# Optimization experiments

Hardware: AMD Instinct MI355X
Metric: run time of the kernel (lower is better)

The kernel has to match this reference:

```python
import jax, jax.numpy as jnp
import numpy as np

B, N, D = 1, 65536, 1024
H = 512
R = 16  # num_regions
C = 2   # num_classes

def _gelu(x):
    return jax.nn.gelu(x, approximate=False)  # torch nn.GELU default is exact erf

def setup_inputs() -> dict:
    key = jax.random.key(0)
    ks = jax.random.split(key, 16)
    s = 0.02
    return {
        "embeddings": jax.random.normal(ks[0], (B, N, D), dtype=jnp.float32),
        # region_encoder: Linear(D,H) + GELU (dropout=0 in eval)
        "W1": jax.random.normal(ks[1], (D, H), dtype=jnp.float32) * s,
        "b1": jnp.zeros((H,), dtype=jnp.float32),
        # region_attention: Linear(H,H//2) -> tanh -> Linear(H//2,1)
        "Wa1": jax.random.normal(ks[2], (H, H // 2), dtype=jnp.float32) * s,
        "ba1": jnp.zeros((H // 2,), dtype=jnp.float32),
        "Wa2": jax.random.normal(ks[3], (H // 2, 1), dtype=jnp.float32) * s,
        "ba2": jnp.zeros((1,), dtype=jnp.float32),
        # slide_encoder: Linear(H,H) + GELU
        "Ws": jax.random.normal(ks[4], (H, H), dtype=jnp.float32) * s,
        "bs": jnp.zeros((H,), dtype=jnp.float32),
        # slide_attention
        "Wsa1": jax.random.normal(ks[5], (H, H // 2), dtype=jnp.float32) * s,
        "bsa1": jnp.zeros((H // 2,), dtype=jnp.float32),
        "Wsa2": jax.random.normal(ks[6], (H // 2, 1), dtype=jnp.float32) * s,
        "bsa2": jnp.zeros((1,), dtype=jnp.float32),
        # classifier: Linear(H,H//2) -> GELU -> Linear(H//2,C)
        "Wc1": jax.random.normal(ks[7], (H, H // 2), dtype=jnp.float32) * s,
        "bc1": jnp.zeros((H // 2,), dtype=jnp.float32),
        "Wc2": jax.random.normal(ks[8], (H // 2, C), dtype=jnp.float32) * s,
        "bc2": jnp.zeros((C,), dtype=jnp.float32),
    }

def reference(embeddings, W1, b1, Wa1, ba1, Wa2, ba2, Ws, bs, Wsa1, bsa1, Wsa2, bsa2, Wc1, bc1, Wc2, bc2):
    b, n, d = embeddings.shape
    m = n // R  # patches per region
    # coords=None path: region_ids[i] = i % R, so region r holds indices r, r+R, ...
    # Equivalent regrouping via reshape+transpose: (B, M, R, D) -> (B, R, M, D)
    x = embeddings.reshape(b, m, R, d).transpose(0, 2, 1, 3)
    # region encoder
    region_emb = _gelu(jnp.einsum('brmd,dh->brmh', x, W1) + b1)  # (B,R,M,H)
    # region attention pooling
    scores = jnp.einsum('brmk,ko->brmo', jnp.tanh(jnp.einsum('brmh,hk->brmk', region_emb, Wa1) + ba1), Wa2) + ba2  # (B,R,M,1)
    attn = jax.nn.softmax(scores, axis=2)
    region_features = jnp.sum(region_emb * attn, axis=2)  # (B,R,H)
    # slide encoder + attention pooling over regions
    slide_emb = _gelu(jnp.einsum('brh,hg->brg', region_features, Ws) + bs)  # (B,R,H)
    sattn = jnp.einsum('brk,ko->bro', jnp.tanh(jnp.einsum('brh,hk->brk', slide_emb, Wsa1) + bsa1), Wsa2) + bsa2  # (B,R,1)
    sweights = jax.nn.softmax(sattn, axis=1)
    slide_rep = jnp.sum(slide_emb * sweights, axis=1)  # (B,H)
    # classifier
    logits = _gelu(slide_rep @ Wc1 + bc1) @ Wc2 + bc2  # (B,C)
    return logits
```

## Files before the change

### kernel.cpp

```cpp
#include <hip/hip_runtime.h>

#define NTOK 65536
#define DIN  1024
#define H    512
#define HH   256
#define NREG 16
#define MPR  4096

__device__ __forceinline__ unsigned short f2bf(float f) {
  unsigned u = __float_as_uint(f);
  u += 0x7fffu + ((u >> 16) & 1u);
  return (unsigned short)(u >> 16);
}
__device__ __forceinline__ float bf2f(unsigned short s) {
  return __uint_as_float(((unsigned)s) << 16);
}
__device__ __forceinline__ float gelu_exact(float x) {
  return 0.5f * x * (1.0f + erff(x * 0.70710678118654752440f));
}

typedef __attribute__((ext_vector_type(8))) short shortx8;
typedef __attribute__((ext_vector_type(4))) float floatx4;

__device__ __forceinline__ void gl_lds16(const void* g, void* l) {
  __builtin_amdgcn_global_load_lds(
      (const __attribute__((address_space(1))) void*)g,
      (__attribute__((address_space(3))) void*)l, 16, 0, 0);
}

__global__ __launch_bounds__(256) void kc_convert(const float* __restrict__ X,
                                                  unsigned short* __restrict__ Xb) {
  size_t i = ((size_t)blockIdx.x * 256 + threadIdx.x) * 8;
  const floatx4* src = (const floatx4*)(X + i);
  floatx4 f0 = src[0], f1 = src[1];
  shortx8 h;
  h[0] = (short)f2bf(f0[0]); h[1] = (short)f2bf(f0[1]);
  h[2] = (short)f2bf(f0[2]); h[3] = (short)f2bf(f0[3]);
  h[4] = (short)f2bf(f1[0]); h[5] = (short)f2bf(f1[1]);
  h[6] = (short)f2bf(f1[2]); h[7] = (short)f2bf(f1[3]);
  *(shortx8*)(Xb + i) = h;
}

__global__ __launch_bounds__(256) void k0_prep(const float* __restrict__ W1,
                                               const float* __restrict__ Wa1,
                                               unsigned short* __restrict__ W1t,
                                               unsigned short* __restrict__ Wa1t) {
  int idx = blockIdx.x * 256 + threadIdx.x;
  if (idx < DIN * H) {
    int n = idx >> 10, k = idx & 1023;
    W1t[idx] = f2bf(W1[k * H + n]);
  } else {
    int i2 = idx - DIN * H;
    int n = i2 >> 9, k = i2 & 511;
    Wa1t[i2] = f2bf(Wa1[k * HH + n]);
  }
}


__global__ __launch_bounds__(256) void k1_gemm1(const unsigned short* __restrict__ Xb,
                                                const unsigned short* __restrict__ W1t,
                                                const float* __restrict__ b1,
                                                unsigned short* __restrict__ Eb) {
  __shared__ __align__(16) short lA[128 * 32];
  __shared__ __align__(16) short lB[128 * 32];
  const int tid = threadIdx.x;
  const int colBase = blockIdx.x * 128;
  const int rowBase = blockIdx.y * 128;
  const int lane = tid & 63;
  const int wave = tid >> 6;
  const int wr = wave >> 1, wc = wave & 1;
  const int l15 = lane & 15, quad = lane >> 4;
  const int sw = (l15 >> 1) & 3;

  floatx4 acc[4][4] = {};

  for (int kb = 0; kb < DIN; kb += 32) {
    __syncthreads();
#pragma unroll
    for (int s = 0; s < 2; s++) {
      int c = tid + s * 256;
      int row = c >> 2;
      int k16g = (c & 3) ^ ((c >> 3) & 3);
      gl_lds16(Xb + (size_t)(rowBase + row) * DIN + kb + k16g * 8, &lA[c * 8]);
      gl_lds16(W1t + (size_t)(colBase + row) * DIN + kb + k16g * 8, &lB[c * 8]);
    }
    __syncthreads();
    shortx8 aF[4], bF[4];
#pragma unroll
    for (int i = 0; i < 4; i++)
      aF[i] = *(const shortx8*)(&lA[(wr * 64 + i * 16 + l15) * 32 + (quad ^ sw) * 8]);
#pragma unroll
    for (int j = 0; j < 4; j++)
      bF[j] = *(const shortx8*)(&lB[(wc * 64 + j * 16 + l15) * 32 + (quad ^ sw) * 8]);
#pragma unroll
    for (int i = 0; i < 4; i++)
#pragma unroll
      for (int j = 0; j < 4; j++)
        acc[i][j] = __builtin_amdgcn_mfma_f32_16x16x32_bf16(aF[i], bF[j], acc[i][j], 0, 0, 0);
  }

  const int row0 = rowBase + wr * 64;
  const int col0 = colBase + wc * 64;
#pragma unroll
  for (int j = 0; j < 4; j++) {
    int col = col0 + j * 16 + l15;
    float bias = b1[col];
#pragma unroll
    for (int i = 0; i < 4; i++) {
      int rb = row0 + i * 16 + quad * 4;
#pragma unroll
      for (int v = 0; v < 4; v++) {
        float x = acc[i][j][v] + bias;
        Eb[(size_t)(rb + v) * H + col] = f2bf(gelu_exact(x));
      }
    }
  }
}

__global__ __launch_bounds__(256) void k2_gemm2(const unsigned short* __restrict__ Eb,
                                                const unsigned short* __restrict__ Wa1t,
                                                const float* __restrict__ ba1,
                                                const float* __restrict__ Wa2,
                                                float* __restrict__ scores) {
  __shared__ __align__(16) short lA[128 * 32];
  __shared__ __align__(16) short lB[128 * 32];
  const int tid = threadIdx.x;
  const int colBase = blockIdx.x * 128;
  const int rowBase = blockIdx.y * 128;
  const int lane = tid & 63;
  const int wave = tid >> 6;
  const int wr = wave >> 1, wc = wave & 1;
  const int l15 = lane & 15, quad = lane >> 4;
  const int sw = (l15 >> 1) & 3;

  floatx4 acc[4][4] = {};

  for (int kb = 0; kb < H; kb += 32) {
    __syncthreads();
#pragma unroll
    for (int s = 0; s < 2; s++) {
      int c = tid + s * 256;
      int row = c >> 2;
      int k16g = (c & 3) ^ ((c >> 3) & 3);
      gl_lds16(Eb + (size_t)(rowBase + row) * H + kb + k16g * 8, &lA[c * 8]);
      gl_lds16(Wa1t + (size_t)(colBase + row) * H + kb + k16g * 8, &lB[c * 8]);
    }
    __syncthreads();
    shortx8 aF[4], bF[4];
#pragma unroll
    for (int i = 0; i < 4; i++)
      aF[i] = *(const shortx8*)(&lA[(wr * 64 + i * 16 + l15) * 32 + (quad ^ sw) * 8]);
#pragma unroll
    for (int j = 0; j < 4; j++)
      bF[j] = *(const shortx8*)(&lB[(wc * 64 + j * 16 + l15) * 32 + (quad ^ sw) * 8]);
#pragma unroll
    for (int i = 0; i < 4; i++)
#pragma unroll
      for (int j = 0; j < 4; j++)
        acc[i][j] = __builtin_amdgcn_mfma_f32_16x16x32_bf16(aF[i], bF[j], acc[i][j], 0, 0, 0);
  }

  float p[4][4];
#pragma unroll
  for (int i = 0; i < 4; i++)
#pragma unroll
    for (int v = 0; v < 4; v++) p[i][v] = 0.0f;
#pragma unroll
  for (int j = 0; j < 4; j++) {
    int col = colBase + wc * 64 + j * 16 + l15;
    float bias = ba1[col];
    float wa2 = Wa2[col];
#pragma unroll
    for (int i = 0; i < 4; i++)
#pragma unroll
      for (int v = 0; v < 4; v++)
        p[i][v] += tanhf(acc[i][j][v] + bias) * wa2;
  }
#pragma unroll
  for (int i = 0; i < 4; i++)
#pragma unroll
    for (int v = 0; v < 4; v++) {
      float t = p[i][v];
      t += __shfl_xor(t, 1, 16);
      t += __shfl_xor(t, 2, 16);
      t += __shfl_xor(t, 4, 16);
      t += __shfl_xor(t, 8, 16);
      p[i][v] = t;
    }
  if (l15 == 0) {
    int row0 = rowBase + wr * 64 + quad * 4;
#pragma unroll
    for (int i = 0; i < 4; i++)
#pragma unroll
      for (int v = 0; v < 4; v++)
        atomicAdd(&scores[row0 + i * 16 + v], p[i][v]);
  }
}

__global__ __launch_bounds__(256) void k3a_softmax(const float* __restrict__ scores,
                                                   float* __restrict__ wts) {
  const int r = blockIdx.x, tid = threadIdx.x;
  __shared__ float red[256];
  float m = -1e30f;
  for (int j = tid; j < MPR; j += 256) m = fmaxf(m, scores[r + NREG * j]);
  red[tid] = m;
  __syncthreads();
  for (int s = 128; s > 0; s >>= 1) {
    if (tid < s) red[tid] = fmaxf(red[tid], red[tid + s]);
    __syncthreads();
  }
  float mx = red[0];
  __syncthreads();
  float sum = 0.0f;
  for (int j = tid; j < MPR; j += 256) sum += expf(scores[r + NREG * j] - mx);
  red[tid] = sum;
  __syncthreads();
  for (int s = 128; s > 0; s >>= 1) {
    if (tid < s) red[tid] += red[tid + s];
    __syncthreads();
  }
  float inv = 1.0f / red[0];
  for (int j = tid; j < MPR; j += 256)
    wts[r + NREG * j] = expf(scores[r + NREG * j] - mx) * inv;
}

__global__ __launch_bounds__(256) void k3b_wsum(const unsigned short* __restrict__ Eb,
                                                const float* __restrict__ wts,
                                                float* __restrict__ rf) {
  const int r = blockIdx.y;
  const int mc = blockIdx.x;
  const int tid = threadIdx.x;
  float a0 = 0.0f, a1 = 0.0f;
  for (int j = mc * 128; j < mc * 128 + 128; j++) {
    int n = r + NREG * j;
    float w = wts[n];
    unsigned v = *(const unsigned*)(Eb + (size_t)n * H + tid * 2);
    a0 += w * bf2f((unsigned short)(v & 0xffffu));
    a1 += w * bf2f((unsigned short)(v >> 16));
  }
  atomicAdd(&rf[r * H + tid * 2], a0);
  atomicAdd(&rf[r * H + tid * 2 + 1], a1);
}

__global__ __launch_bounds__(256) void k4a_slide(const float* __restrict__ rf,
                                                 const float* __restrict__ Ws,
                                                 const float* __restrict__ bs,
                                                 float* __restrict__ se) {
  const int r = blockIdx.x, tid = threadIdx.x;
  __shared__ float lrf[H];
  lrf[tid] = rf[r * H + tid];
  lrf[tid + 256] = rf[r * H + tid + 256];
  __syncthreads();
  float a0 = 0.0f, a1 = 0.0f;
  for (int k = 0; k < H; k++) {
    float x = lrf[k];
    a0 += x * Ws[k * H + tid];
    a1 += x * Ws[k * H + tid + 256];
  }
  se[r * H + tid] = gelu_exact(a0 + bs[tid]);
  se[r * H + tid + 256] = gelu_exact(a1 + bs[tid + 256]);
}

__global__ __launch_bounds__(256) void k4b_sscore(const float* __restrict__ se,
                                                  const float* __restrict__ Wsa1,
                                                  const float* __restrict__ bsa1,
                                                  const float* __restrict__ Wsa2,
                                                  const float* __restrict__ bsa2,
                                                  float* __restrict__ ss) {
  const int r = blockIdx.x, tid = threadIdx.x;
  __shared__ float lse[H];
  __shared__ float red[256];
  lse[tid] = se[r * H + tid];
  lse[tid + 256] = se[r * H + tid + 256];
  __syncthreads();
  float a = 0.0f;
  for (int k = 0; k < H; k++) a += lse[k] * Wsa1[k * HH + tid];
  red[tid] = tanhf(a + bsa1[tid]) * Wsa2[tid];
  __syncthreads();
  for (int s = 128; s > 0; s >>= 1) {
    if (tid < s) red[tid] += red[tid + s];
    __syncthreads();
  }
  if (tid == 0) ss[r] = red[0] + bsa2[0];
}

__global__ __launch_bounds__(256) void k4c_final(const float* __restrict__ se,
                                                 const float* __restrict__ ss,
                                                 const float* __restrict__ Wc1,
                                                 const float* __restrict__ bc1,
                                                 const float* __restrict__ Wc2,
                                                 const float* __restrict__ bc2,
                                                 float* __restrict__ out) {
  const int tid = threadIdx.x;
  __shared__ float srep[H];
  __shared__ float r0[256], r1[256];
  float mx = -1e30f;
  for (int i = 0; i < NREG; i++) mx = fmaxf(mx, ss[i]);
  float wv[NREG];
  float den = 0.0f;
  for (int i = 0; i < NREG; i++) { wv[i] = expf(ss[i] - mx); den += wv[i]; }
  float inv = 1.0f / den;
  float s0 = 0.0f, s1 = 0.0f;
  for (int i = 0; i < NREG; i++) {
    float w = wv[i] * inv;
    s0 += w * se[i * H + tid];
    s1 += w * se[i * H + tid + 256];
  }
  srep[tid] = s0;
  srep[tid + 256] = s1;
  __syncthreads();
  float a = 0.0f;
  for (int k = 0; k < H; k++) a += srep[k] * Wc1[k * HH + tid];
  float g = gelu_exact(a + bc1[tid]);
  r0[tid] = g * Wc2[tid * 2];
  r1[tid] = g * Wc2[tid * 2 + 1];
  __syncthreads();
  for (int s = 128; s > 0; s >>= 1) {
    if (tid < s) { r0[tid] += r0[tid + s]; r1[tid] += r1[tid + s]; }
    __syncthreads();
  }
  if (tid == 0) {
    out[0] = r0[0] + bc2[0];
    out[1] = r1[0] + bc2[1];
  }
}

extern "C" void kernel_launch(void* const* d_in, const int* in_sizes, int n_in,
                              void* d_out, int out_size, void* d_ws, size_t ws_size,
                              hipStream_t stream) {
  const float* X    = (const float*)d_in[0];
  const float* W1   = (const float*)d_in[1];
  const float* b1   = (const float*)d_in[2];
  const float* Wa1  = (const float*)d_in[3];
  const float* ba1  = (const float*)d_in[4];
  const float* Wa2  = (const float*)d_in[5];
  const float* Ws   = (const float*)d_in[7];
  const float* bs   = (const float*)d_in[8];
  const float* Wsa1 = (const float*)d_in[9];
  const float* bsa1 = (const float*)d_in[10];
  const float* Wsa2 = (const float*)d_in[11];
  const float* bsa2 = (const float*)d_in[12];
  const float* Wc1  = (const float*)d_in[13];
  const float* bc1  = (const float*)d_in[14];
  const float* Wc2  = (const float*)d_in[15];
  const float* bc2  = (const float*)d_in[16];
  float* out = (float*)d_out;

  char* ws = (char*)d_ws;
  constexpr size_t OFF_W1T  = 0;
  constexpr size_t OFF_WA1T = OFF_W1T + (size_t)H * DIN * 2;
  constexpr size_t OFF_EB   = OFF_WA1T + (size_t)HH * H * 2;
  constexpr size_t OFF_SC   = OFF_EB + (size_t)NTOK * H * 2;
  constexpr size_t OFF_RF   = OFF_SC + (size_t)NTOK * 4;
  constexpr size_t OFF_WT   = OFF_RF + (size_t)NREG * H * 4;
  constexpr size_t OFF_SE   = OFF_WT + (size_t)NTOK * 4;
  constexpr size_t OFF_SS   = OFF_SE + (size_t)NREG * H * 4;
  constexpr size_t OFF_XB   = OFF_SS + 256;

  unsigned short* W1t  = (unsigned short*)(ws + OFF_W1T);
  unsigned short* Wa1t = (unsigned short*)(ws + OFF_WA1T);
  unsigned short* Eb   = (unsigned short*)(ws + OFF_EB);
  float* scores = (float*)(ws + OFF_SC);
  float* rf     = (float*)(ws + OFF_RF);
  float* wts    = (float*)(ws + OFF_WT);
  float* se     = (float*)(ws + OFF_SE);
  float* ssb    = (float*)(ws + OFF_SS);
  unsigned short* Xb = (unsigned short*)(ws + OFF_XB);

  hipMemsetAsync(scores, 0, (size_t)NTOK * 4 + (size_t)NREG * H * 4, stream);

  kc_convert<<<(NTOK * (size_t)DIN / 8 + 255) / 256, 256, 0, stream>>>(X, Xb);
  k0_prep<<<(DIN * H + HH * H) / 256, 256, 0, stream>>>(W1, Wa1, W1t, Wa1t);
  k1_gemm1<<<dim3(4, 512), 256, 0, stream>>>(Xb, W1t, b1, Eb);
  k2_gemm2<<<dim3(2, 512), 256, 0, stream>>>(Eb, Wa1t, ba1, Wa2, scores);
  k3a_softmax<<<NREG, 256, 0, stream>>>(scores, wts);
  k3b_wsum<<<dim3(32, NREG), 256, 0, stream>>>(Eb, wts, rf);
  k4a_slide<<<NREG, 256, 0, stream>>>(rf, Ws, bs, se);
  k4b_sscore<<<NREG, 256, 0, stream>>>(se, Wsa1, bsa1, Wsa2, bsa2, ssb);
  k4c_final<<<1, 256, 0, stream>>>(se, ssb, Wc1, bc1, Wc2, bc2, out);
}
```

Measured before the change: 670.0 us.

## Fuse region-encoder and attention GEMMs per row tile, use fast GELU/tanh

Merges the two big GEMM kernels into one kernel where each block owns 128 rows. It computes all 512 hidden columns, writes them to the Eb buffer, then immediately re-reads its own rows for the attention GEMM. The scores are reduced in LDS and written directly, so the atomics and most of the memset go away. It also doubles the K tile to 64 with a new swizzle, fuses the slide encoder with slide scoring, and replaces erf/tanh with polynomial and exp approximations. The grid drops to 512 blocks, which reduces parallelism. The approximate GELU adds small numeric error.

```diff
diff --git a/kernel.cpp b/kernel.cpp
--- a/kernel.cpp
+++ b/kernel.cpp
@@ -15,8 +15,18 @@
 __device__ __forceinline__ float bf2f(unsigned short s) {
   return __uint_as_float(((unsigned)s) << 16);
 }
-__device__ __forceinline__ float gelu_exact(float x) {
-  return 0.5f * x * (1.0f + erff(x * 0.70710678118654752440f));
+__device__ __forceinline__ float gelu_fast(float x) {
+  float ax = fabsf(x) * 0.70710678118654752f;
+  float t  = 1.0f / fmaf(0.3275911f, ax, 1.0f);
+  float poly = t * fmaf(t, fmaf(t, fmaf(t, fmaf(t, 1.061405429f, -1.453152027f),
+                                        1.421413741f), -0.284496736f), 0.254829592f);
+  float erfv = fmaf(-poly, __expf(-ax * ax), 1.0f);
+  float s = (x >= 0.0f) ? erfv : -erfv;
+  return 0.5f * x * (1.0f + s);
+}
+__device__ __forceinline__ float tanh_fast(float x) {
+  float e = __expf(2.0f * x);
+  return 1.0f - 2.0f / (e + 1.0f);
 }
 
 typedef __attribute__((ext_vector_type(8))) short shortx8;
@@ -57,124 +67,118 @@
 }
 
 
-__global__ __launch_bounds__(256) void k1_gemm1(const unsigned short* __restrict__ Xb,
-                                                const unsigned short* __restrict__ W1t,
-                                                const float* __restrict__ b1,
-                                                unsigned short* __restrict__ Eb) {
-  __shared__ __align__(16) short lA[128 * 32];
-  __shared__ __align__(16) short lB[128 * 32];
+__global__ __launch_bounds__(256) void k12_fused(const unsigned short* __restrict__ Xb,
+                                                 const unsigned short* __restrict__ W1t,
+                                                 const float* __restrict__ b1,
+                                                 const unsigned short* __restrict__ Wa1t,
+                                                 const float* __restrict__ ba1,
+                                                 const float* __restrict__ Wa2,
+                                                 unsigned short* __restrict__ Eb,
+                                                 float* __restrict__ scores) {
+  __shared__ __align__(16) short lA[128 * 64];
+  __shared__ __align__(16) short lB[128 * 64];
+  __shared__ float scomb[256];
   const int tid = threadIdx.x;
-  const int colBase = blockIdx.x * 128;
-  const int rowBase = blockIdx.y * 128;
+  const int rowBase = blockIdx.x * 128;
   const int lane = tid & 63;
   const int wave = tid >> 6;
   const int wr = wave >> 1, wc = wave & 1;
   const int l15 = lane & 15, quad = lane >> 4;
-  const int sw = (l15 >> 1) & 3;
-
-  floatx4 acc[4][4] = {};
-
-  for (int kb = 0; kb < DIN; kb += 32) {
-    __syncthreads();
-#pragma unroll
-    for (int s = 0; s < 2; s++) {
-      int c = tid + s * 256;
-      int row = c >> 2;
-      int k16g = (c & 3) ^ ((c >> 3) & 3);
-      gl_lds16(Xb + (size_t)(rowBase + row) * DIN + kb + k16g * 8, &lA[c * 8]);
-      gl_lds16(W1t + (size_t)(colBase + row) * DIN + kb + k16g * 8, &lB[c * 8]);
-    }
-    __syncthreads();
-    shortx8 aF[4], bF[4];
-#pragma unroll
-    for (int i = 0; i < 4; i++)
-      aF[i] = *(const shortx8*)(&lA[(wr * 64 + i * 16 + l15) * 32 + (quad ^ sw) * 8]);
-#pragma unroll
-    for (int j = 0; j < 4; j++)
-      bF[j] = *(const shortx8*)(&lB[(wc * 64 + j * 16 + l15) * 32 + (quad ^ sw) * 8]);
-#pragma unroll
-    for (int i = 0; i < 4; i++)
-#pragma unroll
-      for (int j = 0; j < 4; j++)
-        acc[i][j] = __builtin_amdgcn_mfma_f32_16x16x32_bf16(aF[i], bF[j], acc[i][j], 0, 0, 0);
-  }
-
-  const int row0 = rowBase + wr * 64;
-  const int col0 = colBase + wc * 64;
-#pragma unroll
-  for (int j = 0; j < 4; j++) {
-    int col = col0 + j * 16 + l15;
-    float bias = b1[col];
-#pragma unroll
-    for (int i = 0; i < 4; i++) {
-      int rb = row0 + i * 16 + quad * 4;
-#pragma unroll
-      for (int v = 0; v < 4; v++) {
-        float x = acc[i][j][v] + bias;
-        Eb[(size_t)(rb + v) * H + col] = f2bf(gelu_exact(x));
-      }
-    }
-  }
-}
-
-__global__ __launch_bounds__(256) void k2_gemm2(const unsigned short* __restrict__ Eb,
-                                                const unsigned short* __restrict__ Wa1t,
-                                                const float* __restrict__ ba1,
-                                                const float* __restrict__ Wa2,
-                                                float* __restrict__ scores) {
-  __shared__ __align__(16) short lA[128 * 32];
-  __shared__ __align__(16) short lB[128 * 32];
-  const int tid = threadIdx.x;
-  const int colBase = blockIdx.x * 128;
-  const int rowBase = blockIdx.y * 128;
-  const int lane = tid & 63;
-  const int wave = tid >> 6;
-  const int wr = wave >> 1, wc = wave & 1;
-  const int l15 = lane & 15, quad = lane >> 4;
-  const int sw = (l15 >> 1) & 3;
-
-  floatx4 acc[4][4] = {};
-
-  for (int kb = 0; kb < H; kb += 32) {
-    __syncthreads();
-#pragma unroll
-    for (int s = 0; s < 2; s++) {
-      int c = tid + s * 256;
-      int row = c >> 2;
-      int k16g = (c & 3) ^ ((c >> 3) & 3);
-      gl_lds16(Eb + (size_t)(rowBase + row) * H + kb + k16g * 8, &lA[c * 8]);
-      gl_lds16(Wa1t + (size_t)(colBase + row) * H + kb + k16g * 8, &lB[c * 8]);
-    }
-    __syncthreads();
-    shortx8 aF[4], bF[4];
-#pragma unroll
-    for (int i = 0; i < 4; i++)
-      aF[i] = *(const shortx8*)(&lA[(wr * 64 + i * 16 + l15) * 32 + (quad ^ sw) * 8]);
-#pragma unroll
-    for (int j = 0; j < 4; j++)
-      bF[j] = *(const shortx8*)(&lB[(wc * 64 + j * 16 + l15) * 32 + (quad ^ sw) * 8]);
-#pragma unroll
-    for (int i = 0; i < 4; i++)
-#pragma unroll
-      for (int j = 0; j < 4; j++)
-        acc[i][j] = __builtin_amdgcn_mfma_f32_16x16x32_bf16(aF[i], bF[j], acc[i][j], 0, 0, 0);
-  }
+  const int rsw = l15 & 7;
+
+  for (int ct = 0; ct < 4; ct++) {
+    floatx4 acc[4][4] = {};
+    for (int kb = 0; kb < DIN; kb += 64) {
+      __syncthreads();
+#pragma unroll
+      for (int s = 0; s < 4; s++) {
+        int c = tid + s * 256;
+        int row = c >> 3;
+        int kc_ = (c & 7) ^ (row & 7);
+        gl_lds16(Xb + (size_t)(rowBase + row) * DIN + kb + kc_ * 8, &lA[c * 8]);
+        gl_lds16(W1t + (size_t)(ct * 128 + row) * DIN + kb + kc_ * 8, &lB[c * 8]);
+      }
+      __syncthreads();
+#pragma unroll
+      for (int h = 0; h < 2; h++) {
+        shortx8 aF[4], bF[4];
+#pragma unroll
+        for (int i = 0; i < 4; i++)
+          aF[i] = *(const shortx8*)(&lA[(wr * 64 + i * 16 + l15) * 64 + (((h << 2) + quad) ^ rsw) * 8]);
+#pragma unroll
+        for (int j = 0; j < 4; j++)
+          bF[j] = *(const shortx8*)(&lB[(wc * 64 + j * 16 + l15) * 64 + (((h << 2) + quad) ^ rsw) * 8]);
+#pragma unroll
+        for (int i = 0; i < 4; i++)
+#pragma unroll
+          for (int j = 0; j < 4; j++)
+            acc[i][j] = __builtin_amdgcn_mfma_f32_16x16x32_bf16(aF[i], bF[j], acc[i][j], 0, 0, 0);
+      }
+    }
+    const int row0 = rowBase + wr * 64;
+    const int col0 = ct * 128 + wc * 64;
+#pragma unroll
+    for (int j = 0; j < 4; j++) {
+      int col = col0 + j * 16 + l15;
+      float bias = b1[col];
+#pragma unroll
+      for (int i = 0; i < 4; i++) {
+        int rb = row0 + i * 16 + quad * 4;
+#pragma unroll
+        for (int v = 0; v < 4; v++)
+          Eb[(size_t)(rb + v) * H + col] = f2bf(gelu_fast(acc[i][j][v] + bias));
+      }
+    }
+  }
+
+  __threadfence();
 
   float p[4][4];
 #pragma unroll
   for (int i = 0; i < 4; i++)
 #pragma unroll
     for (int v = 0; v < 4; v++) p[i][v] = 0.0f;
-#pragma unroll
-  for (int j = 0; j < 4; j++) {
-    int col = colBase + wc * 64 + j * 16 + l15;
-    float bias = ba1[col];
-    float wa2 = Wa2[col];
-#pragma unroll
-    for (int i = 0; i < 4; i++)
-#pragma unroll
-      for (int v = 0; v < 4; v++)
-        p[i][v] += tanhf(acc[i][j][v] + bias) * wa2;
+
+  for (int n2 = 0; n2 < 2; n2++) {
+    floatx4 acc[4][4] = {};
+    for (int kb = 0; kb < H; kb += 64) {
+      __syncthreads();
+#pragma unroll
+      for (int s = 0; s < 4; s++) {
+        int c = tid + s * 256;
+        int row = c >> 3;
+        int kc_ = (c & 7) ^ (row & 7);
+        gl_lds16(Eb + (size_t)(rowBase + row) * H + kb + kc_ * 8, &lA[c * 8]);
+        gl_lds16(Wa1t + (size_t)(n2 * 128 + row) * H + kb + kc_ * 8, &lB[c * 8]);
+      }
+      __syncthreads();
+#pragma unroll
+      for (int h = 0; h < 2; h++) {
+        shortx8 aF[4], bF[4];
+#pragma unroll
+        for (int i = 0; i < 4; i++)
+          aF[i] = *(const shortx8*)(&lA[(wr * 64 + i * 16 + l15) * 64 + (((h << 2) + quad) ^ rsw) * 8]);
+#pragma unroll
+        for (int j = 0; j < 4; j++)
+          bF[j] = *(const shortx8*)(&lB[(wc * 64 + j * 16 + l15) * 64 + (((h << 2) + quad) ^ rsw) * 8]);
+#pragma unroll
+        for (int i = 0; i < 4; i++)
+#pragma unroll
+          for (int j = 0; j < 4; j++)
+            acc[i][j] = __builtin_amdgcn_mfma_f32_16x16x32_bf16(aF[i], bF[j], acc[i][j], 0, 0, 0);
+      }
+    }
+#pragma unroll
+    for (int j = 0; j < 4; j++) {
+      int col = n2 * 128 + wc * 64 + j * 16 + l15;
+      float bias = ba1[col];
+      float wa2 = Wa2[col];
+#pragma unroll
+      for (int i = 0; i < 4; i++)
+#pragma unroll
+        for (int v = 0; v < 4; v++)
+          p[i][v] += tanh_fast(acc[i][j][v] + bias) * wa2;
+    }
   }
 #pragma unroll
   for (int i = 0; i < 4; i++)
@@ -187,14 +191,16 @@
       t += __shfl_xor(t, 8, 16);
       p[i][v] = t;
     }
+  __syncthreads();
   if (l15 == 0) {
-    int row0 = rowBase + wr * 64 + quad * 4;
 #pragma unroll
     for (int i = 0; i < 4; i++)
 #pragma unroll
       for (int v = 0; v < 4; v++)
-        atomicAdd(&scores[row0 + i * 16 + v], p[i][v]);
-  }
+        scomb[(wr * 64 + i * 16 + quad * 4 + v) * 2 + wc] = p[i][v];
+  }
+  __syncthreads();
+  if (tid < 128) scores[rowBase + tid] = scomb[tid * 2] + scomb[tid * 2 + 1];
 }
 
 __global__ __launch_bounds__(256) void k3a_softmax(const float* __restrict__ scores,
@@ -242,12 +248,19 @@
   atomicAdd(&rf[r * H + tid * 2 + 1], a1);
 }
 
-__global__ __launch_bounds__(256) void k4a_slide(const float* __restrict__ rf,
-                                                 const float* __restrict__ Ws,
-                                                 const float* __restrict__ bs,
-                                                 float* __restrict__ se) {
+__global__ __launch_bounds__(256) void k4ab_slide(const float* __restrict__ rf,
+                                                  const float* __restrict__ Ws,
+                                                  const float* __restrict__ bs,
+                                                  const float* __restrict__ Wsa1,
+                                                  const float* __restrict__ bsa1,
+                                                  const float* __restrict__ Wsa2,
+                                                  const float* __restrict__ bsa2,
+                                                  float* __restrict__ se,
+                                                  float* __restrict__ ss) {
   const int r = blockIdx.x, tid = threadIdx.x;
   __shared__ float lrf[H];
+  __shared__ float lse[H];
+  __shared__ float red[256];
   lrf[tid] = rf[r * H + tid];
   lrf[tid + 256] = rf[r * H + tid + 256];
   __syncthreads();
@@ -257,25 +270,16 @@
     a0 += x * Ws[k * H + tid];
     a1 += x * Ws[k * H + tid + 256];
   }
-  se[r * H + tid] = gelu_exact(a0 + bs[tid]);
-  se[r * H + tid + 256] = gelu_exact(a1 + bs[tid + 256]);
-}
-
-__global__ __launch_bounds__(256) void k4b_sscore(const float* __restrict__ se,
-                                                  const float* __restrict__ Wsa1,
-                                                  const float* __restrict__ bsa1,
-                                                  const float* __restrict__ Wsa2,
-                                                  const float* __restrict__ bsa2,
-                                                  float* __restrict__ ss) {
-  const int r = blockIdx.x, tid = threadIdx.x;
-  __shared__ float lse[H];
-  __shared__ float red[256];
-  lse[tid] = se[r * H + tid];
-  lse[tid + 256] = se[r * H + tid + 256];
+  float s0 = gelu_fast(a0 + bs[tid]);
+  float s1 = gelu_fast(a1 + bs[tid + 256]);
+  se[r * H + tid] = s0;
+  se[r * H + tid + 256] = s1;
+  lse[tid] = s0;
+  lse[tid + 256] = s1;
   __syncthreads();
   float a = 0.0f;
   for (int k = 0; k < H; k++) a += lse[k] * Wsa1[k * HH + tid];
-  red[tid] = tanhf(a + bsa1[tid]) * Wsa2[tid];
+  red[tid] = tanh_fast(a + bsa1[tid]) * Wsa2[tid];
   __syncthreads();
   for (int s = 128; s > 0; s >>= 1) {
     if (tid < s) red[tid] += red[tid + s];
@@ -311,7 +315,7 @@
   __syncthreads();
   float a = 0.0f;
   for (int k = 0; k < H; k++) a += srep[k] * Wc1[k * HH + tid];
-  float g = gelu_exact(a + bc1[tid]);
+  float g = gelu_fast(a + bc1[tid]);
   r0[tid] = g * Wc2[tid * 2];
   r1[tid] = g * Wc2[tid * 2 + 1];
   __syncthreads();
@@ -367,15 +371,13 @@
   float* ssb    = (float*)(ws + OFF_SS);
   unsigned short* Xb = (unsigned short*)(ws + OFF_XB);
 
-  hipMemsetAsync(scores, 0, (size_t)NTOK * 4 + (size_t)NREG * H * 4, stream);
+  hipMemsetAsync(rf, 0, (size_t)NREG * H * 4, stream);
 
   kc_convert<<<(NTOK * (size_t)DIN / 8 + 255) / 256, 256, 0, stream>>>(X, Xb);
   k0_prep<<<(DIN * H + HH * H) / 256, 256, 0, stream>>>(W1, Wa1, W1t, Wa1t);
-  k1_gemm1<<<dim3(4, 512), 256, 0, stream>>>(Xb, W1t, b1, Eb);
-  k2_gemm2<<<dim3(2, 512), 256, 0, stream>>>(Eb, Wa1t, ba1, Wa2, scores);
+  k12_fused<<<512, 256, 0, stream>>>(Xb, W1t, b1, Wa1t, ba1, Wa2, Eb, scores);
   k3a_softmax<<<NREG, 256, 0, stream>>>(scores, wts);
   k3b_wsum<<<dim3(32, NREG), 256, 0, stream>>>(Eb, wts, rf);
-  k4a_slide<<<NREG, 256, 0, stream>>>(rf, Ws, bs, se);
-  k4b_sscore<<<NREG, 256, 0, stream>>>(se, Wsa1, bsa1, Wsa2, bsa2, ssb);
+  k4ab_slide<<<NREG, 256, 0, stream>>>(rf, Ws, bs, Wsa1, bsa1, Wsa2, bsa2, se, ssb);
   k4c_final<<<1, 256, 0, stream>>>(se, ssb, Wc1, bc1, Wc2, bc2, out);
 }
```

Measured after the change: 815.0 us. +21.6%, slower.
